# Performance work log

Hardware: AMD Instinct MI355X
Metric: run time of the kernel (lower is better)

## Reference

```python
import jax, jax.numpy as jnp
import numpy as np

T, B, D, H = 512, 8, 512, 8
DH = D // H


def _sinusoidal(pos, dim):
    # pos: (t, t) float relative distances -> (t, t, dim)
    half = dim // 2
    freqs = jnp.exp(-jnp.log(10000.0) * jnp.arange(half, dtype=jnp.float32) / half)
    ang = pos[..., None] * freqs  # (t, t, half)
    return jnp.concatenate([jnp.sin(ang), jnp.cos(ang)], axis=-1)


def setup_inputs() -> dict:
    key = jax.random.key(0)
    ks = jax.random.split(key, 7)
    s = 0.02
    return {
        "x": jax.random.normal(ks[0], (T, B, D), jnp.float32),
        "W_qkv": jax.random.normal(ks[1], (D, 3 * D), jnp.float32) * s,  # to_qkv (no bias)
        "W_pos": jax.random.normal(ks[2], (D, D), jnp.float32) * s,      # to_pos (no bias)
        "pos_u": jax.random.normal(ks[3], (H, DH), jnp.float32),
        "pos_v": jax.random.normal(ks[4], (H, DH), jnp.float32),
        "W_out": jax.random.normal(ks[5], (D, D), jnp.float32) * s,
        "b_out": jnp.zeros((D,), jnp.float32),
        "log_one_div_by_tau": jnp.zeros((1,), jnp.float32),
    }


def reference(x, W_qkv, W_pos, pos_u, pos_v, W_out, b_out, log_one_div_by_tau):
    t, b, d = x.shape
    h, dh = pos_u.shape
    scale = dh ** (-0.5)

    qkv = x @ W_qkv                                   # (t, b, 3d)
    q, k, v = jnp.split(qkv, 3, axis=-1)
    q = q.reshape(t, b, h, dh)
    k = k.reshape(t, b, h, dh)
    v = v.reshape(t, b, h, dh)

    # relative position embeddings
    seq = jnp.arange(t, dtype=jnp.float32)
    rel_dist = seq[:, None] - seq[None, :]            # (t, t)
    rpe = _sinusoidal(rel_dist, d) @ W_pos            # (t, t, d)
    rpe = rpe.reshape(t, t, h, dh)

    # Transformer-XL energy: AC + BD + global content bias + global pos bias
    energy = (
        jnp.einsum('ibhd,jbhd->ijbh', q, k)
        + jnp.einsum('ibhd,ijhd->ijbh', q, rpe)
        + jnp.einsum('hd,jbhd->jbh', pos_u, k)[None, :, :, :]
        + jnp.einsum('hd,ijhd->ijh', pos_v, rpe)[:, :, None, :]
    )
    energy = energy * scale

    # diag mask
    diag = jnp.eye(t, dtype=bool)[:, :, None, None]
    energy = jnp.where(diag, -jnp.finfo(energy.dtype).max, energy)

    # log temperature
    energy = energy * jnp.exp(log_one_div_by_tau)

    attn = jax.nn.softmax(energy, axis=1)             # softmax over j
    out = jnp.einsum('ijbh,jbhd->ibhd', attn, v).reshape(t, b, d)
    return out @ W_out + b_out
```

## Files before the change

### kernel.cpp

```cpp
#include <hip/hip_runtime.h>
#include <hip/hip_bf16.h>

#define TT 512
#define BB 8
#define DD 512
#define HH 8
#define DHH 64

typedef unsigned short ushort_t;
using frag16 = __attribute__((ext_vector_type(8))) short;
using f32x4  = __attribute__((ext_vector_type(4))) float;
using usx4   = __attribute__((ext_vector_type(4))) ushort_t;

#define MFMA16 __builtin_amdgcn_mfma_f32_16x16x32_bf16

__device__ inline ushort_t f2bf(float x) {
    __hip_bfloat16 h = __float2bfloat16(x);
    ushort_t u; __builtin_memcpy(&u, &h, 2); return u;
}
__device__ inline float bf2f(ushort_t u) {
    __hip_bfloat16 h; __builtin_memcpy(&h, &u, 2);
    return __bfloat162float(h);
}

__device__ inline void gload16(const void* g, void* l) {
    __builtin_amdgcn_global_load_lds(
        (const __attribute__((address_space(1))) unsigned int*)g,
        (__attribute__((address_space(3))) unsigned int*)l, 16, 0, 0);
}

__device__ inline void split_t_tile(const float* __restrict__ in,
                                    ushort_t* __restrict__ oh,
                                    ushort_t* __restrict__ ol,
                                    int K, int N, int bx, int by, int tid,
                                    float (*tile)[33]) {
    int n0 = bx * 32, k0 = by * 32;
    {
        int r = tid >> 3, c0 = (tid & 7) * 4;
        float4 v = *(const float4*)&in[(size_t)(k0 + r) * N + n0 + c0];
        tile[r][c0] = v.x; tile[r][c0 + 1] = v.y;
        tile[r][c0 + 2] = v.z; tile[r][c0 + 3] = v.w;
    }
    __syncthreads();
    {
        int n = tid >> 3, kk = (tid & 7) * 4;
        usx4 H, L;
        #pragma unroll
        for (int t = 0; t < 4; ++t) {
            float x = tile[kk + t][n];
            ushort_t hh = f2bf(x);
            H[t] = hh;
            L[t] = f2bf(x - bf2f(hh));
        }
        *(usx4*)&oh[(size_t)(n0 + n) * K + k0 + kk] = H;
        *(usx4*)&ol[(size_t)(n0 + n) * K + k0 + kk] = L;
    }
}

__global__ __launch_bounds__(256) void prep_kernel(
        const float* __restrict__ x, const float* __restrict__ W_pos,
        const float* __restrict__ W_qkv, const float* __restrict__ W_out,
        ushort_t* __restrict__ fh, ushort_t* __restrict__ fl,
        ushort_t* __restrict__ xh,
        ushort_t* __restrict__ WposT_h, ushort_t* __restrict__ WposT_l,
        ushort_t* __restrict__ WqkvT_h, ushort_t* __restrict__ WqkvT_l,
        ushort_t* __restrict__ WoutT_h, ushort_t* __restrict__ WoutT_l) {
    __shared__ float tile[32][33];
    int blk = blockIdx.x;
    int tid = threadIdx.x;
    if (blk < 512) {
        int idx = blk * 1024 + tid * 4;
        int r = idx >> 9, c0 = idx & 511;
        float dist = (float)(r - 511);
        const float nl4 = -logf(10000.0f) / 256.0f;
        usx4 H, L;
        #pragma unroll
        for (int t = 0; t < 4; ++t) {
            int c = c0 + t;
            int cc = c & 255;
            float freq = __expf(nl4 * (float)cc);
            float ang = dist * freq;
            float v = (c < 256) ? __sinf(ang) : __cosf(ang);
            ushort_t hh = f2bf(v);
            H[t] = hh;
            L[t] = f2bf(v - bf2f(hh));
        }
        *(usx4*)&fh[idx] = H;
        *(usx4*)&fl[idx] = L;
    } else if (blk < 2560) {
        int i = (blk - 512) * 256 + tid;
        float4 v = ((const float4*)x)[i];
        float e[4] = {v.x, v.y, v.z, v.w};
        usx4 H;
        #pragma unroll
        for (int t = 0; t < 4; ++t) H[t] = f2bf(e[t]);
        ((usx4*)xh)[i] = H;
    } else if (blk < 2816) {
        int f = blk - 2560;
        split_t_tile(W_pos, WposT_h, WposT_l, 512, 512, f & 15, f >> 4, tid, tile);
    } else if (blk < 3584) {
        int f = blk - 2816;
        split_t_tile(W_qkv, WqkvT_h, WqkvT_l, 512, 1536, f % 48, f / 48, tid, tile);
    } else {
        int f = blk - 3584;
        split_t_tile(W_out, WoutT_h, WoutT_l, 512, 512, f & 15, f >> 4, tid, tile);
    }
}

template <int TM, int TN, int MODE, int APL, int BK, int BPL>
__device__ void gemm_bf3_dev(
        ushort_t* lds0, ushort_t* lds1, int bx, int by,
        const ushort_t* __restrict__ Ah, const ushort_t* __restrict__ Al,
        const ushort_t* __restrict__ Bh, const ushort_t* __restrict__ Bl,
        const float* __restrict__ bias, float* __restrict__ C,
        ushort_t* __restrict__ Ch, ushort_t* __restrict__ Cl,
        int M, int N, int K, int lo_nlim) {
    constexpr int NMI = TM / 32;
    constexpr int NNI = TN / 32;
    constexpr int CHK = BK / 8;
    constexpr int ACELLS = APL * CHK * TM;
    constexpr int BCELLS = BPL * CHK * TN;
    constexpr int NCH = (ACELLS + BCELLS) / 64;

    const int tid = threadIdx.x;
    const int lane = tid & 63;
    const int w = tid >> 6;
    const int wm = w & 1, wn = w >> 1;
    const int c = lane & 15, quad = lane >> 4;
    const int m0 = by * TM;
    const int n0 = bx * TN;
    const bool wlo = (MODE == 1) && (BPL == 2) && (n0 < lo_nlim);

    auto stage = [&](int k0, ushort_t* lds) {
        #pragma unroll
        for (int ci = 0; ci < NCH / 4; ++ci) {
            int ch = ci * 4 + w;
            int cell = ch * 64 + lane;
            const ushort_t* src;
            if (cell < ACELLS) {
                int plane = cell / (CHK * TM);
                int rem = cell - plane * CHK * TM;
                int q = rem / TM, r = rem - q * TM;
                src = (plane ? Al : Ah) + (size_t)(m0 + r) * K + k0 + q * 8;
            } else {
                int cb = cell - ACELLS;
                int plane = (BPL == 2) ? (cb / (CHK * TN)) : 0;
                int rem = cb - plane * CHK * TN;
                int q = rem / TN, r = rem - q * TN;
                src = (plane ? Bl : Bh) + (size_t)(n0 + r) * K + k0 + q * 8;
            }
            gload16(src, &lds[(size_t)(ch * 64) * 8]);
        }
    };

    f32x4 acc[NMI][NNI];
    #pragma unroll
    for (int mi = 0; mi < NMI; ++mi)
        #pragma unroll
        for (int ni = 0; ni < NNI; ++ni)
            acc[mi][ni] = (f32x4){0.f, 0.f, 0.f, 0.f};

    const int NIT = K / BK;
    stage(0, lds0);
    for (int it = 0; it < NIT; ++it) {
        ushort_t* cur = (it & 1) ? lds1 : lds0;
        ushort_t* nxt = (it & 1) ? lds0 : lds1;
        __syncthreads();
        if (it + 1 < NIT) stage((it + 1) * BK, nxt);

        #pragma unroll
        for (int ks = 0; ks < BK / 32; ++ks) {
            frag16 a_h[NMI], a_l[NMI], b_h[NNI], b_l[NNI];
            #pragma unroll
            for (int mi = 0; mi < NMI; ++mi) {
                int arow = wm * (TM / 2) + mi * 16 + c;
                a_h[mi] = *(const frag16*)&cur[((ks * 4 + quad) * TM + arow) * 8];
                if (APL == 2)
                    a_l[mi] = *(const frag16*)&cur[((CHK + ks * 4 + quad) * TM + arow) * 8];
            }
            #pragma unroll
            for (int ni = 0; ni < NNI; ++ni) {
                int brow = wn * (TN / 2) + ni * 16 + c;
                b_h[ni] = *(const frag16*)&cur[(ACELLS + (ks * 4 + quad) * TN + brow) * 8];
                if (BPL == 2)
                    b_l[ni] = *(const frag16*)&cur[(ACELLS + (CHK + ks * 4 + quad) * TN + brow) * 8];
            }
            #pragma unroll
            for (int mi = 0; mi < NMI; ++mi)
                #pragma unroll
                for (int ni = 0; ni < NNI; ++ni) {
                    acc[mi][ni] = MFMA16(a_h[mi], b_h[ni], acc[mi][ni], 0, 0, 0);
                    if (BPL == 2)
                        acc[mi][ni] = MFMA16(a_h[mi], b_l[ni], acc[mi][ni], 0, 0, 0);
                    if (APL == 2)
                        acc[mi][ni] = MFMA16(a_l[mi], b_h[ni], acc[mi][ni], 0, 0, 0);
                }
        }
    }

    if constexpr (MODE == 3) {
        __syncthreads();
        ushort_t* tp = lds0;
        #pragma unroll
        for (int mi = 0; mi < NMI; ++mi)
            #pragma unroll
            for (int ni = 0; ni < NNI; ++ni)
                #pragma unroll
                for (int reg = 0; reg < 4; ++reg) {
                    int lm = wm * (TM / 2) + mi * 16 + quad * 4 + reg;
                    int ln = wn * (TN / 2) + ni * 16 + c;
                    tp[lm * 136 + ln] = f2bf(acc[mi][ni][reg]);
                }
        __syncthreads();
        int t0 = m0 >> 3;
        #pragma unroll
        for (int rr = 0; rr < 4; ++rr) {
            int row = tid + rr * 256;
            int bloc = row >> 7, dl = row & 127;
            union { frag16 v; ushort_t s[8]; } P0, P1;
            #pragma unroll
            for (int tl = 0; tl < 8; ++tl)
                P0.s[tl] = tp[(tl * 8 + bloc) * 136 + dl];
            #pragma unroll
            for (int tl = 0; tl < 8; ++tl)
                P1.s[tl] = tp[((tl + 8) * 8 + bloc) * 136 + dl];
            size_t dst = ((size_t)bloc * DD + (n0 - 1024) + dl) * TT + t0;
            *(frag16*)&Ch[dst]     = P0.v;
            *(frag16*)&Ch[dst + 8] = P1.v;
        }
        return;
    }

    #pragma unroll
    for (int mi = 0; mi < NMI; ++mi)
        #pragma unroll
        for (int ni = 0; ni < NNI; ++ni)
            #pragma unroll
            for (int reg = 0; reg < 4; ++reg) {
                int gm = m0 + wm * (TM / 2) + mi * 16 + quad * 4 + reg;
                int gn = n0 + wn * (TN / 2) + ni * 16 + c;
                float v = acc[mi][ni][reg];
                if (MODE == 0) {
                    C[(size_t)gm * N + gn] = v + bias[gn];
                } else {
                    ushort_t hh = f2bf(v);
                    Ch[(size_t)gm * N + gn] = hh;
                    if (MODE == 1 && wlo)
                        Cl[(size_t)gm * N + gn] = f2bf(v - bf2f(hh));
                }
            }
}

__global__ __launch_bounds__(256, 2) void big_gemm(
        const ushort_t* __restrict__ x_h,
        const ushort_t* __restrict__ WqkvT_h, const ushort_t* __restrict__ WqkvT_l,
        ushort_t* __restrict__ qkv_h, ushort_t* __restrict__ qkv_l,
        ushort_t* __restrict__ vt_h,
        const ushort_t* __restrict__ feat_h, const ushort_t* __restrict__ feat_l,
        const ushort_t* __restrict__ WposT_h, const ushort_t* __restrict__ WposT_l,
        ushort_t* __restrict__ table_h) {
    __shared__ __align__(16) ushort_t lds[2 * 16384];
    int blk = blockIdx.x;
    if (blk < 384) {
        int xcd = blk & 7, idx = blk >> 3;
        int bm = xcd * 4 + idx / 12;
        int bn = idx % 12;
        if (bn < 4) {
            gemm_bf3_dev<128, 128, 1, 1, 32, 2>(lds, lds + 12288, bn, bm,
                                                x_h, nullptr, WqkvT_h, WqkvT_l,
                                                nullptr, nullptr, qkv_h, qkv_l,
                                                4096, 1536, 512, 512);
        } else if (bn < 8) {
            gemm_bf3_dev<128, 128, 1, 1, 32, 1>(lds, lds + 8192, bn, bm,
                                                x_h, nullptr, WqkvT_h, nullptr,
                                                nullptr, nullptr, qkv_h, qkv_l,
                                                4096, 1536, 512, 512);
        } else {
            gemm_bf3_dev<128, 128, 3, 1, 32, 1>(lds, lds + 8192, bn, bm,
                                                x_h, nullptr, WqkvT_h, nullptr,
                                                nullptr, nullptr, vt_h, nullptr,
                                                4096, 1536, 512, 0);
        }
    } else {
        int f = blk - 384;
        int xcd = f & 7, idx = f >> 3;
        int bm = xcd * 2 + (idx >> 3);
        int bn = idx & 7;
        gemm_bf3_dev<64, 64, 2, 2, 64, 2>(lds, lds + 16384, bn, bm,
                                          feat_h, feat_l, WposT_h, WposT_l,
                                          nullptr, nullptr, table_h, nullptr,
                                          1024, 512, 512, 0);
    }
}

__global__ __launch_bounds__(256, 2) void outproj_gemm(
        const ushort_t* __restrict__ ao_h, const ushort_t* __restrict__ ao_l,
        const ushort_t* __restrict__ WoutT_h, const ushort_t* __restrict__ WoutT_l,
        const float* __restrict__ bias, float* __restrict__ C) {
    __shared__ __align__(16) ushort_t lds[2 * 16384];
    int blk = blockIdx.x;
    int xcd = blk & 7, idx = blk >> 3;
    int bm = xcd * 8 + (idx >> 3);
    int bn = idx & 7;
    gemm_bf3_dev<64, 64, 0, 2, 64, 2>(lds, lds + 16384, bn, bm,
                                      ao_h, ao_l, WoutT_h, WoutT_l,
                                      bias, C, nullptr, nullptr,
                                      4096, 512, 512, 0);
}

struct WU {
    union {
        float    qp[16][81];
        ushort_t p[16][72];
    };
};

__global__ __launch_bounds__(256, 2) void attn_kernel(
        const ushort_t* __restrict__ qkv_h, const ushort_t* __restrict__ qkv_l,
        const ushort_t* __restrict__ T_h,
        const ushort_t* __restrict__ vt_h,
        const float* __restrict__ pos_u, const float* __restrict__ pos_v,
        const float* __restrict__ tau,
        ushort_t* __restrict__ o_h, ushort_t* __restrict__ o_l) {
    const int b  = blockIdx.x;
    const int i0 = blockIdx.y * 64;
    const int h  = blockIdx.z;
    const int tid  = threadIdx.x;
    const int lane = tid & 63;
    const int w    = tid >> 6;
    const int c    = lane & 15;
    const int quad = lane >> 4;

    __shared__ __align__(16) ushort_t Kbuf[2][4096];
    __shared__ __align__(16) ushort_t Vbuf[2][4096];
    __shared__ __align__(16) ushort_t Pbuf[192 * 64];
    __shared__ __align__(16) WU wbuf[4];

    const int chl = (lane & 7) ^ (lane >> 3);
    const int rql = lane >> 3;
    const int swz0 = quad ^ (c & 7);
    const int swz1 = (4 + quad) ^ (c & 7);

    const float tauexp = expf(tau[0]);
    const float scale  = 0.125f;
    const float NEGMAX = -3.4028234663852886e38f;

    frag16 qu_h[2], qu_l[2], qv_h[2], qv_l[2];
    {
        int row = i0 + w * 16 + c;
        size_t base = ((size_t)row * BB + b) * (3 * DD) + h * DHH;
        const float* up = pos_u + h * DHH;
        const float* vp = pos_v + h * DHH;
        #pragma unroll
        for (int kb = 0; kb < 2; ++kb) {
            int d0 = kb * 32 + quad * 8;
            union { frag16 v; ushort_t s[8]; } QH, QL, UH, UL, VH, VL;
            QH.v = *(const frag16*)&qkv_h[base + d0];
            QL.v = *(const frag16*)&qkv_l[base + d0];
            #pragma unroll
            for (int t = 0; t < 8; ++t) {
                float q = bf2f(QH.s[t]) + bf2f(QL.s[t]);
                float a = q + up[d0 + t];
                ushort_t ah = f2bf(a);
                UH.s[t] = ah; UL.s[t] = f2bf(a - bf2f(ah));
                float bq = q + vp[d0 + t];
                ushort_t bh = f2bf(bq);
                VH.s[t] = bh; VL.s[t] = f2bf(bq - bf2f(bh));
            }
            qu_h[kb] = UH.v; qu_l[kb] = UL.v;
            qv_h[kb] = VH.v; qv_l[kb] = VL.v;
        }
    }

    auto stageKV = [&](int jt) {
        const int j0 = jt * 64;
        ushort_t* kb = Kbuf[jt & 1];
        ushort_t* vb = Vbuf[jt & 1];
        #pragma unroll
        for (int it = 0; it < 2; ++it) {
            int r0 = (it * 4 + w) * 8;
            const ushort_t* src = qkv_h
                + ((size_t)(j0 + r0 + rql) * BB + b) * (3 * DD) + DD + h * DHH + chl * 8;
            gload16(src, &kb[r0 * 64]);
        }
        #pragma unroll
        for (int it = 0; it < 2; ++it) {
            int r0 = (it * 4 + w) * 8;
            const ushort_t* src = vt_h
                + ((size_t)b * DD + h * DHH + r0 + rql) * TT + j0 + chl * 8;
            gload16(src, &vb[r0 * 64]);
        }
    };
    auto stageP = [&](int rowbase, int slotbase, int nit) {
        for (int it = 0; it < nit; ++it) {
            int off = (it * 4 + w) * 8;
            int sbase = slotbase + off;
            if (sbase >= 192) sbase -= 192;
            const ushort_t* src = T_h + (size_t)(rowbase + off + rql) * DD + h * DHH + chl * 8;
            gload16(src, &Pbuf[sbase * 64]);
        }
    };

    float m_r[4], l_r[4];
    f32x4 o_acc[4];
    #pragma unroll
    for (int r = 0; r < 4; ++r) { m_r[r] = NEGMAX; l_r[r] = 0.f; }
    #pragma unroll
    for (int d = 0; d < 4; ++d) o_acc[d] = (f32x4){0.f, 0.f, 0.f, 0.f};

    int rmod = (i0 + 448) % 192;
    stageKV(0);
    stageP(i0 + 448, rmod, 4);

    for (int jt = 0; jt < 8; ++jt) {
        const int j0  = jt * 64;
        const int rlo = i0 - j0 + 448;
        const int rmodN = (rmod >= 64) ? rmod - 64 : rmod + 128;

        __syncthreads();

        if (jt + 1 < 8) {
            stageKV(jt + 1);
            stageP(rlo - 64, rmodN, 2);
        }
        const ushort_t* kbc = Kbuf[jt & 1];
        const ushort_t* vbc = Vbuf[jt & 1];

        f32x4 qp_acc[5];
        __builtin_amdgcn_s_setprio(1);
        #pragma unroll
        for (int rs = 0; rs < 5; ++rs) {
            f32x4 acc = (f32x4){0.f, 0.f, 0.f, 0.f};
            int slot = rmod + w * 16 + rs * 16 + c;
            if (slot >= 192) slot -= 192;
            frag16 p0 = *(const frag16*)&Pbuf[slot * 64 + swz0 * 8];
            frag16 p1 = *(const frag16*)&Pbuf[slot * 64 + swz1 * 8];
            acc = MFMA16(qv_h[0], p0, acc, 0, 0, 0);
            acc = MFMA16(qv_l[0], p0, acc, 0, 0, 0);
            acc = MFMA16(qv_h[1], p1, acc, 0, 0, 0);
            acc = MFMA16(qv_l[1], p1, acc, 0, 0, 0);
            qp_acc[rs] = acc;
        }
        __builtin_amdgcn_s_setprio(0);
        #pragma unroll
        for (int rs = 0; rs < 5; ++rs)
            #pragma unroll
            for (int reg = 0; reg < 4; ++reg)
                wbuf[w].qp[quad * 4 + reg][rs * 16 + c] = qp_acc[rs][reg];

        f32x4 ac[4];
        __builtin_amdgcn_s_setprio(1);
        #pragma unroll
        for (int js = 0; js < 4; ++js) {
            f32x4 acc = (f32x4){0.f, 0.f, 0.f, 0.f};
            int krow = js * 16 + c;
            frag16 kh0 = *(const frag16*)&kbc[krow * 64 + swz0 * 8];
            frag16 kh1 = *(const frag16*)&kbc[krow * 64 + swz1 * 8];
            acc = MFMA16(qu_h[0], kh0, acc, 0, 0, 0);
            acc = MFMA16(qu_l[0], kh0, acc, 0, 0, 0);
            acc = MFMA16(qu_h[1], kh1, acc, 0, 0, 0);
            acc = MFMA16(qu_l[1], kh1, acc, 0, 0, 0);
            ac[js] = acc;
        }
        __builtin_amdgcn_s_setprio(0);

        float ev[4][4];
        #pragma unroll
        for (int js = 0; js < 4; ++js) {
            int jl = js * 16 + c;
            #pragma unroll
            for (int reg = 0; reg < 4; ++reg) {
                int il = quad * 4 + reg;
                float bd = wbuf[w].qp[il][il - jl + 63];
                float e = (ac[js][reg] + bd) * scale;
                if (i0 + w * 16 + il == j0 + jl) e = NEGMAX;
                ev[js][reg] = e * tauexp;
            }
        }

        float alpha[4], mn[4];
        #pragma unroll
        for (int reg = 0; reg < 4; ++reg) {
            float mx = fmaxf(fmaxf(ev[0][reg], ev[1][reg]),
                             fmaxf(ev[2][reg], ev[3][reg]));
            #pragma unroll
            for (int m = 1; m < 16; m <<= 1) mx = fmaxf(mx, __shfl_xor(mx, m));
            float m2 = fmaxf(m_r[reg], mx);
            alpha[reg] = __expf(m_r[reg] - m2);
            mn[reg] = m2;
            m_r[reg] = m2;
        }
        float ss[4] = {0.f, 0.f, 0.f, 0.f};
        #pragma unroll
        for (int js = 0; js < 4; ++js) {
            int jl = js * 16 + c;
            #pragma unroll
            for (int reg = 0; reg < 4; ++reg) {
                float p = __expf(ev[js][reg] - mn[reg]);
                ushort_t ph = f2bf(p);
                ss[reg] += bf2f(ph);
                wbuf[w].p[quad * 4 + reg][jl] = ph;
            }
        }
        #pragma unroll
        for (int reg = 0; reg < 4; ++reg) {
            float s = ss[reg];
            #pragma unroll
            for (int m = 1; m < 16; m <<= 1) s += __shfl_xor(s, m);
            l_r[reg] = l_r[reg] * alpha[reg] + s;
        }

        frag16 pf0 = *(const frag16*)&wbuf[w].p[c][quad * 8];
        frag16 pf1 = *(const frag16*)&wbuf[w].p[c][32 + quad * 8];
        __builtin_amdgcn_s_setprio(1);
        #pragma unroll
        for (int ds = 0; ds < 4; ++ds) {
            f32x4 acc = o_acc[ds];
            #pragma unroll
            for (int reg = 0; reg < 4; ++reg) acc[reg] *= alpha[reg];
            int vrow = ds * 16 + c;
            frag16 vh0 = *(const frag16*)&vbc[vrow * 64 + swz0 * 8];
            frag16 vh1 = *(const frag16*)&vbc[vrow * 64 + swz1 * 8];
            acc = MFMA16(pf0, vh0, acc, 0, 0, 0);
            acc = MFMA16(pf1, vh1, acc, 0, 0, 0);
            o_acc[ds] = acc;
        }
        __builtin_amdgcn_s_setprio(0);

        rmod = rmodN;
    }

    #pragma unroll
    for (int reg = 0; reg < 4; ++reg)
        l_r[reg] = __builtin_amdgcn_rcpf(l_r[reg]);
    #pragma unroll
    for (int ds = 0; ds < 4; ++ds)
        #pragma unroll
        for (int reg = 0; reg < 4; ++reg) {
            int row = i0 + w * 16 + quad * 4 + reg;
            size_t idx = ((size_t)row * BB + b) * DD + h * DHH + ds * 16 + c;
            float val = o_acc[ds][reg] * l_r[reg];
            ushort_t hh = f2bf(val);
            o_h[idx] = hh;
            o_l[idx] = f2bf(val - bf2f(hh));
        }
}

extern "C" void kernel_launch(void* const* d_in, const int* in_sizes, int n_in,
                              void* d_out, int out_size, void* d_ws, size_t ws_size,
                              hipStream_t stream) {
    const float* x     = (const float*)d_in[0];
    const float* W_qkv = (const float*)d_in[1];
    const float* W_pos = (const float*)d_in[2];
    const float* pos_u = (const float*)d_in[3];
    const float* pos_v = (const float*)d_in[4];
    const float* W_out = (const float*)d_in[5];
    const float* b_out = (const float*)d_in[6];
    const float* tau   = (const float*)d_in[7];
    float* out = (float*)d_out;

    ushort_t* p = (ushort_t*)d_ws;
    ushort_t* feat_h  = p; p += 1024 * 512;
    ushort_t* feat_l  = p; p += 1024 * 512;
    ushort_t* WposT_h = p; p += 512 * 512;
    ushort_t* WposT_l = p; p += 512 * 512;
    ushort_t* table_h = p; p += 1024 * 512;
    ushort_t* x_h     = p; p += 4096 * 512;
    ushort_t* WqkvT_h = p; p += 1536 * 512;
    ushort_t* WqkvT_l = p; p += 1536 * 512;
    ushort_t* qkv_h   = p; p += 4096 * 1536;
    ushort_t* qkv_l   = p; p += 4096 * 1536;
    ushort_t* WoutT_h = p; p += 512 * 512;
    ushort_t* WoutT_l = p; p += 512 * 512;
    ushort_t* ao_h    = p; p += 4096 * 512;
    ushort_t* ao_l    = p; p += 4096 * 512;
    ushort_t* vt_h    = p; p += BB * DD * TT;

    prep_kernel<<<3840, 256, 0, stream>>>(
        x, W_pos, W_qkv, W_out, feat_h, feat_l, x_h,
        WposT_h, WposT_l, WqkvT_h, WqkvT_l, WoutT_h, WoutT_l);
    big_gemm<<<512, 256, 0, stream>>>(
        x_h, WqkvT_h, WqkvT_l, qkv_h, qkv_l, vt_h,
        feat_h, feat_l, WposT_h, WposT_l, table_h);
    attn_kernel<<<dim3(BB, 8, HH), 256, 0, stream>>>(
        qkv_h, qkv_l, table_h, vt_h, pos_u, pos_v, tau, ao_h, ao_l);
    outproj_gemm<<<512, 256, 0, stream>>>(
        ao_h, ao_l, WoutT_h, WoutT_l, b_out, out);
}
```

Baseline: 148.8 us.

## Drop low-order bf16 split terms for Q and positional features; transpose qp scratch

Removes the low-part bf16 plane for the sinusoidal features and for the q+u / q+v operands in attention. This halves the MFMAs in the QK and Q·P products and skips computing and writing the features' low plane. The per-warp qp scratch is also transposed to [80][18] so stores become 2-wide vector writes and diagonal reads index differently. Accuracy drops because those operands now carry only bf16 precision instead of a hi+lo split.

```diff
diff --git a/kernel.cpp b/kernel.cpp
--- a/kernel.cpp
+++ b/kernel.cpp
@@ -10,6 +10,7 @@
 typedef unsigned short ushort_t;
 using frag16 = __attribute__((ext_vector_type(8))) short;
 using f32x4  = __attribute__((ext_vector_type(4))) float;
+using f32x2  = __attribute__((ext_vector_type(2))) float;
 using usx4   = __attribute__((ext_vector_type(4))) ushort_t;
 
 #define MFMA16 __builtin_amdgcn_mfma_f32_16x16x32_bf16
@@ -73,7 +74,7 @@
         int r = idx >> 9, c0 = idx & 511;
         float dist = (float)(r - 511);
         const float nl4 = -logf(10000.0f) / 256.0f;
-        usx4 H, L;
+        usx4 H;
         #pragma unroll
         for (int t = 0; t < 4; ++t) {
             int c = c0 + t;
@@ -81,12 +82,9 @@
             float freq = __expf(nl4 * (float)cc);
             float ang = dist * freq;
             float v = (c < 256) ? __sinf(ang) : __cosf(ang);
-            ushort_t hh = f2bf(v);
-            H[t] = hh;
-            L[t] = f2bf(v - bf2f(hh));
+            H[t] = f2bf(v);
         }
         *(usx4*)&fh[idx] = H;
-        *(usx4*)&fl[idx] = L;
     } else if (blk < 2560) {
         int i = (blk - 512) * 256 + tid;
         float4 v = ((const float4*)x)[i];
@@ -138,7 +136,7 @@
             int cell = ch * 64 + lane;
             const ushort_t* src;
             if (cell < ACELLS) {
-                int plane = cell / (CHK * TM);
+                int plane = (APL == 2) ? (cell / (CHK * TM)) : 0;
                 int rem = cell - plane * CHK * TM;
                 int q = rem / TM, r = rem - q * TM;
                 src = (plane ? Al : Ah) + (size_t)(m0 + r) * K + k0 + q * 8;
@@ -256,7 +254,7 @@
         const ushort_t* __restrict__ WqkvT_h, const ushort_t* __restrict__ WqkvT_l,
         ushort_t* __restrict__ qkv_h, ushort_t* __restrict__ qkv_l,
         ushort_t* __restrict__ vt_h,
-        const ushort_t* __restrict__ feat_h, const ushort_t* __restrict__ feat_l,
+        const ushort_t* __restrict__ feat_h,
         const ushort_t* __restrict__ WposT_h, const ushort_t* __restrict__ WposT_l,
         ushort_t* __restrict__ table_h) {
     __shared__ __align__(16) ushort_t lds[2 * 16384];
@@ -286,8 +284,8 @@
         int xcd = f & 7, idx = f >> 3;
         int bm = xcd * 2 + (idx >> 3);
         int bn = idx & 7;
-        gemm_bf3_dev<64, 64, 2, 2, 64, 2>(lds, lds + 16384, bn, bm,
-                                          feat_h, feat_l, WposT_h, WposT_l,
+        gemm_bf3_dev<64, 64, 2, 1, 64, 2>(lds, lds + 12288, bn, bm,
+                                          feat_h, nullptr, WposT_h, WposT_l,
                                           nullptr, nullptr, table_h, nullptr,
                                           1024, 512, 512, 0);
     }
@@ -310,7 +308,7 @@
 
 struct WU {
     union {
-        float    qp[16][81];
+        float    qp[80][18];
         ushort_t p[16][72];
     };
 };
@@ -345,7 +343,7 @@
     const float scale  = 0.125f;
     const float NEGMAX = -3.4028234663852886e38f;
 
-    frag16 qu_h[2], qu_l[2], qv_h[2], qv_l[2];
+    frag16 qu_h[2], qv_h[2];
     {
         int row = i0 + w * 16 + c;
         size_t base = ((size_t)row * BB + b) * (3 * DD) + h * DHH;
@@ -354,21 +352,17 @@
         #pragma unroll
         for (int kb = 0; kb < 2; ++kb) {
             int d0 = kb * 32 + quad * 8;
-            union { frag16 v; ushort_t s[8]; } QH, QL, UH, UL, VH, VL;
+            union { frag16 v; ushort_t s[8]; } QH, QL, UH, VH;
             QH.v = *(const frag16*)&qkv_h[base + d0];
             QL.v = *(const frag16*)&qkv_l[base + d0];
             #pragma unroll
             for (int t = 0; t < 8; ++t) {
                 float q = bf2f(QH.s[t]) + bf2f(QL.s[t]);
-                float a = q + up[d0 + t];
-                ushort_t ah = f2bf(a);
-                UH.s[t] = ah; UL.s[t] = f2bf(a - bf2f(ah));
-                float bq = q + vp[d0 + t];
-                ushort_t bh = f2bf(bq);
-                VH.s[t] = bh; VL.s[t] = f2bf(bq - bf2f(bh));
-            }
-            qu_h[kb] = UH.v; qu_l[kb] = UL.v;
-            qv_h[kb] = VH.v; qv_l[kb] = VL.v;
+                UH.s[t] = f2bf(q + up[d0 + t]);
+                VH.s[t] = f2bf(q + vp[d0 + t]);
+            }
+            qu_h[kb] = UH.v;
+            qv_h[kb] = VH.v;
         }
     }
 
@@ -436,17 +430,17 @@
             frag16 p0 = *(const frag16*)&Pbuf[slot * 64 + swz0 * 8];
             frag16 p1 = *(const frag16*)&Pbuf[slot * 64 + swz1 * 8];
             acc = MFMA16(qv_h[0], p0, acc, 0, 0, 0);
-            acc = MFMA16(qv_l[0], p0, acc, 0, 0, 0);
             acc = MFMA16(qv_h[1], p1, acc, 0, 0, 0);
-            acc = MFMA16(qv_l[1], p1, acc, 0, 0, 0);
             qp_acc[rs] = acc;
         }
         __builtin_amdgcn_s_setprio(0);
         #pragma unroll
-        for (int rs = 0; rs < 5; ++rs)
-            #pragma unroll
-            for (int reg = 0; reg < 4; ++reg)
-                wbuf[w].qp[quad * 4 + reg][rs * 16 + c] = qp_acc[rs][reg];
+        for (int rs = 0; rs < 5; ++rs) {
+            f32x2 lo2 = (f32x2){qp_acc[rs][0], qp_acc[rs][1]};
+            f32x2 hi2 = (f32x2){qp_acc[rs][2], qp_acc[rs][3]};
+            *(f32x2*)&wbuf[w].qp[rs * 16 + c][quad * 4]     = lo2;
+            *(f32x2*)&wbuf[w].qp[rs * 16 + c][quad * 4 + 2] = hi2;
+        }
 
         f32x4 ac[4];
         __builtin_amdgcn_s_setprio(1);
@@ -457,9 +451,7 @@
             frag16 kh0 = *(const frag16*)&kbc[krow * 64 + swz0 * 8];
             frag16 kh1 = *(const frag16*)&kbc[krow * 64 + swz1 * 8];
             acc = MFMA16(qu_h[0], kh0, acc, 0, 0, 0);
-            acc = MFMA16(qu_l[0], kh0, acc, 0, 0, 0);
             acc = MFMA16(qu_h[1], kh1, acc, 0, 0, 0);
-            acc = MFMA16(qu_l[1], kh1, acc, 0, 0, 0);
             ac[js] = acc;
         }
         __builtin_amdgcn_s_setprio(0);
@@ -471,7 +463,7 @@
             #pragma unroll
             for (int reg = 0; reg < 4; ++reg) {
                 int il = quad * 4 + reg;
-                float bd = wbuf[w].qp[il][il - jl + 63];
+                float bd = wbuf[w].qp[il - jl + 63][il];
                 float e = (ac[js][reg] + bd) * scale;
                 if (i0 + w * 16 + il == j0 + jl) e = NEGMAX;
                 ev[js][reg] = e * tauexp;
@@ -581,7 +573,7 @@
         WposT_h, WposT_l, WqkvT_h, WqkvT_l, WoutT_h, WoutT_l);
     big_gemm<<<512, 256, 0, stream>>>(
         x_h, WqkvT_h, WqkvT_l, qkv_h, qkv_l, vt_h,
-        feat_h, feat_l, WposT_h, WposT_l, table_h);
+        feat_h, WposT_h, WposT_l, table_h);
     attn_kernel<<<dim3(BB, 8, HH), 256, 0, stream>>>(
         qkv_h, qkv_l, table_h, vt_h, pos_u, pos_v, tau, ao_h, ao_l);
     outproj_gemm<<<512, 256, 0, stream>>>(
```

After: 147.5 us. Within noise of the previous version (-0.9%).
